# Kernel optimization log

Hardware: AMD Instinct MI355X
Metric: run time of the kernel (lower is better)

Reference implementation:

```python
import jax, jax.numpy as jnp
import numpy as np

ROI_SIZE = 7
N_ROIS = 64
H = W = 16
C = 2048


def _crop_resize(fm, box):
    """Crop fm[y1:y2, x1:x2] and bilinear-resize (TF2 half-pixel) to [S,S,C].
    fm: [H,W,C], box: [4] = (x1,y1,x2,y2) floats."""
    Hf, Wf = float(fm.shape[0]), float(fm.shape[1])
    S = ROI_SIZE
    x1 = jnp.maximum(0.0, jnp.round(box[0]))
    y1 = jnp.maximum(0.0, jnp.round(box[1]))
    x2 = jnp.minimum(Wf - 1.0, jnp.round(box[2]))
    y2 = jnp.minimum(Hf - 1.0, jnp.round(box[3]))
    h = y2 - y1  # crop is fm[y1:y2], i.e. height h
    w = x2 - x1
    # TF2 bilinear resize: half-pixel centers, coords relative to the crop
    iy = (jnp.arange(S, dtype=jnp.float32) + 0.5) * h / S - 0.5
    ix = (jnp.arange(S, dtype=jnp.float32) + 0.5) * w / S - 0.5
    iy = jnp.clip(iy, 0.0, h - 1.0)
    ix = jnp.clip(ix, 0.0, w - 1.0)
    y0 = jnp.floor(iy)
    x0 = jnp.floor(ix)
    fy = (iy - y0)[:, None, None]  # [S,1,1]
    fx = (ix - x0)[None, :, None]  # [1,S,1]
    y0i = (y1 + y0).astype(jnp.int32)
    y1i = jnp.minimum(y0i + 1, (y1 + h - 1.0).astype(jnp.int32))
    x0i = (x1 + x0).astype(jnp.int32)
    x1i = jnp.minimum(x0i + 1, (x1 + w - 1.0).astype(jnp.int32))
    top = jnp.take(fm, y0i, axis=0)   # [S,W,C]
    bot = jnp.take(fm, y1i, axis=0)
    rows = top * (1.0 - fy) + bot * fy
    left = jnp.take(rows, x0i, axis=1)   # [S,S,C]
    right = jnp.take(rows, x1i, axis=1)
    return left * (1.0 - fx) + right * fx


def setup_inputs() -> dict:
    key = jax.random.key(0)
    ks = jax.random.split(key, 8)
    feature_map = jax.random.normal(ks[0], (1, H, W, C), dtype=jnp.float32)
    # valid boxes: x1,y1 in [0,8), width/height in [2,7)
    lo = jax.random.uniform(ks[1], (N_ROIS, 2), minval=0.0, maxval=8.0)
    span = jax.random.uniform(ks[2], (N_ROIS, 2), minval=2.0, maxval=7.0)
    proposals = jnp.concatenate([lo, lo + span], axis=1)  # (x1,y1,x2,y2)
    D = ROI_SIZE * ROI_SIZE * C  # 100352
    W1 = jax.random.normal(ks[3], (D, 1024), dtype=jnp.float32) * 0.01
    b1 = jnp.zeros((1024,), jnp.float32)
    W2 = jax.random.normal(ks[4], (1024, 1024), dtype=jnp.float32) * 0.02
    b2 = jnp.zeros((1024,), jnp.float32)
    Wc = jax.random.normal(ks[5], (1024, 2), dtype=jnp.float32) * 0.02
    bc = jnp.zeros((2,), jnp.float32)
    Wb = jax.random.normal(ks[6], (1024, 4), dtype=jnp.float32) * 0.02
    bb = jnp.zeros((4,), jnp.float32)
    return {"feature_map": feature_map, "proposals": proposals,
            "W1": W1, "b1": b1, "W2": W2, "b2": b2,
            "Wc": Wc, "bc": bc, "Wb": Wb, "bb": bb}


def reference(feature_map, proposals, W1, b1, W2, b2, Wc, bc, Wb, bb):
    fm = feature_map[0]  # [H,W,C]
    rois = jax.vmap(lambda b: _crop_resize(fm, b))(proposals)  # [N,S,S,C]
    x = rois.reshape(proposals.shape[0], -1)                   # [N, S*S*C]
    x = jax.nn.relu(x @ W1 + b1)
    x = jax.nn.relu(x @ W2 + b2)
    cls_score = jax.nn.softmax(x @ Wc + bc, axis=-1)
    bbox_pred = x @ Wb + bb
    return cls_score, bbox_pred
```

## Files before the change

### kernel.cpp

```cpp
#include <hip/hip_runtime.h>
#include <math.h>

#define SS 7
#define NROIS 64
#define CC 2048
#define DD (SS*SS*CC)
#define MM 64
#define NN 1024
#define NP1 256
#define KC2 16
#define KCH2 64
#define W1COLS 512
#define WSTRIDE 520
#define FC1_LDS (32 * WSTRIDE * 4)

typedef float f32x4 __attribute__((ext_vector_type(4)));
typedef __bf16 bf16x8 __attribute__((ext_vector_type(8)));

#define LDS_BARRIER() do {                                         \
    asm volatile("s_waitcnt lgkmcnt(0)" ::: "memory");             \
    __builtin_amdgcn_s_barrier();                                  \
} while (0)

__device__ __forceinline__ unsigned short f2bf(float f){
    unsigned u = __builtin_bit_cast(unsigned, f);
    u += 0x7fffu + ((u >> 16) & 1u);
    return (unsigned short)(u >> 16);
}
__device__ __forceinline__ float bf2f(unsigned short h){
    unsigned u = ((unsigned)h) << 16;
    return __builtin_bit_cast(float, u);
}
__device__ __forceinline__ void splitpk(float v0, float v1, unsigned& h, unsigned& l){
    __bf16 h0 = (__bf16)v0, h1 = (__bf16)v1;
    float r0 = v0 - (float)h0, r1 = v1 - (float)h1;
    __bf16 l0 = (__bf16)r0, l1 = (__bf16)r1;
    h = (unsigned)__builtin_bit_cast(unsigned short, h0) |
        ((unsigned)__builtin_bit_cast(unsigned short, h1) << 16);
    l = (unsigned)__builtin_bit_cast(unsigned short, l0) |
        ((unsigned)__builtin_bit_cast(unsigned short, l1) << 16);
}


__global__ void crop_kernel(const float* __restrict__ fm,
                            const float* __restrict__ boxes,
                            unsigned short* __restrict__ XI) {
    int roi = blockIdx.x;
    int p   = blockIdx.y;
    int sy = p / SS, sx = p % SS;
    const float* b = boxes + roi * 4;
    float x1 = fmaxf(0.f, rintf(b[0]));
    float y1 = fmaxf(0.f, rintf(b[1]));
    float x2 = fminf(15.f, rintf(b[2]));
    float y2 = fminf(15.f, rintf(b[3]));
    float h = y2 - y1, w = x2 - x1;
    float iy = ((sy + 0.5f) * h) / 7.0f - 0.5f;
    float ix = ((sx + 0.5f) * w) / 7.0f - 0.5f;
    iy = fminf(fmaxf(iy, 0.f), h - 1.f);
    ix = fminf(fmaxf(ix, 0.f), w - 1.f);
    float y0 = floorf(iy), x0 = floorf(ix);
    float fy = iy - y0,   fx = ix - x0;
    int y0i = (int)(y1 + y0);
    int y1i = min(y0i + 1, (int)(y1 + h - 1.f));
    int x0i = (int)(x1 + x0);
    int x1i = min(x0i + 1, (int)(x1 + w - 1.f));

    int c = threadIdx.x * 4;
    const float4 v00 = *(const float4*)(fm + ((size_t)(y0i*16 + x0i))*CC + c);
    const float4 v01 = *(const float4*)(fm + ((size_t)(y0i*16 + x1i))*CC + c);
    const float4 v10 = *(const float4*)(fm + ((size_t)(y1i*16 + x0i))*CC + c);
    const float4 v11 = *(const float4*)(fm + ((size_t)(y1i*16 + x1i))*CC + c);
    float gy = 1.f - fy, gx = 1.f - fx;
    float o[4];
    o[0] = (v00.x*gy + v10.x*fy)*gx + (v01.x*gy + v11.x*fy)*fx;
    o[1] = (v00.y*gy + v10.y*fy)*gx + (v01.y*gy + v11.y*fy)*fx;
    o[2] = (v00.z*gy + v10.z*fy)*gx + (v01.z*gy + v11.z*fy)*fx;
    o[3] = (v00.w*gy + v10.w*fy)*gx + (v01.w*gy + v11.w*fy)*fx;
    uint2 hv, lv;
    splitpk(o[0], o[1], hv.x, lv.x);
    splitpk(o[2], o[3], hv.y, lv.y);
    int k = p * CC + c;
    size_t off = (size_t)roi * (2*DD) + (size_t)(k >> 3) * 16 + (k & 7);
    *(uint2*)(XI + off)     = hv;
    *(uint2*)(XI + off + 8) = lv;
}

__global__ __launch_bounds__(256, 2)
void fc1_gld(const unsigned short* __restrict__ AI,
             const float* __restrict__ Wm, float* __restrict__ P) {
    const int kc = blockIdx.x;
    const int nb = blockIdx.y;
    const int kt_cnt = 12 + (kc < 64 ? 1 : 0);
    const int k0 = (kc * 12 + (kc < 64 ? kc : 64)) * 32;

    const int t = threadIdx.x;
    const int lane = t & 63, wv = t >> 6;
    const int ln = lane & 15;
    const int koff = (lane >> 4) * 8;

    extern __shared__ float WS[];

    f32x4 acc[32];
    #pragma unroll
    for (int i = 0; i < 32; ++i) acc[i] = (f32x4){0.f, 0.f, 0.f, 0.f};

    size_t abase[4];
    #pragma unroll
    for (int mf = 0; mf < 4; ++mf)
        abase[mf] = (size_t)(mf * 16 + ln) * (2*DD) + (size_t)(k0 + koff) * 2;

    bf16x8 Ah[4], Al[4];

    const float* wtile = Wm + (size_t)k0 * NN + nb * W1COLS;

    for (int kt = 0; kt < kt_cnt; ++kt) {
        {
            const float* g0 = wtile + ((size_t)kt * 32 + wv * 8) * NN + (lane << 2);
            #pragma unroll
            for (int rr = 0; rr < 8; ++rr) {
                const float* g = g0 + (size_t)rr * NN;
                float* l = WS + (wv * 8 + rr) * WSTRIDE;
                __builtin_amdgcn_global_load_lds(
                    (const __attribute__((address_space(1))) void*)g,
                    (__attribute__((address_space(3))) void*)l, 16, 0, 0);
                __builtin_amdgcn_global_load_lds(
                    (const __attribute__((address_space(1))) void*)(g + 256),
                    (__attribute__((address_space(3))) void*)(l + 256), 16, 0, 0);
            }
        }
        #pragma unroll
        for (int mf = 0; mf < 4; ++mf) {
            Ah[mf] = *(const bf16x8*)(AI + abase[mf] + (size_t)kt * 64);
            Al[mf] = *(const bf16x8*)(AI + abase[mf] + (size_t)kt * 64 + 8);
        }
        __syncthreads();
        #pragma unroll
        for (int nf = 0; nf < 8; ++nf) {
            const int cb = koff * WSTRIDE + wv * 128 + nf * 16 + ln;
            float f0 = WS[cb + 0*WSTRIDE];
            float f1 = WS[cb + 1*WSTRIDE];
            float f2 = WS[cb + 2*WSTRIDE];
            float f3 = WS[cb + 3*WSTRIDE];
            float f4 = WS[cb + 4*WSTRIDE];
            float f5 = WS[cb + 5*WSTRIDE];
            float f6 = WS[cb + 6*WSTRIDE];
            float f7 = WS[cb + 7*WSTRIDE];
            unsigned h01,l01,h23,l23,h45,l45,h67,l67;
            splitpk(f0, f1, h01, l01);
            splitpk(f2, f3, h23, l23);
            splitpk(f4, f5, h45, l45);
            splitpk(f6, f7, h67, l67);
            typedef unsigned int uintx4 __attribute__((ext_vector_type(4)));
            bf16x8 Bh = __builtin_bit_cast(bf16x8, (uintx4){h01, h23, h45, h67});
            bf16x8 Bl = __builtin_bit_cast(bf16x8, (uintx4){l01, l23, l45, l67});
            #pragma unroll
            for (int mf = 0; mf < 4; ++mf) {
                acc[nf*4+mf] = __builtin_amdgcn_mfma_f32_16x16x32_bf16(Ah[mf], Bh, acc[nf*4+mf], 0, 0, 0);
                acc[nf*4+mf] = __builtin_amdgcn_mfma_f32_16x16x32_bf16(Ah[mf], Bl, acc[nf*4+mf], 0, 0, 0);
                acc[nf*4+mf] = __builtin_amdgcn_mfma_f32_16x16x32_bf16(Al[mf], Bh, acc[nf*4+mf], 0, 0, 0);
            }
        }
        __syncthreads();
    }

    const int orb = (lane >> 4) * 4;
    #pragma unroll
    for (int nf = 0; nf < 8; ++nf) {
        int col = nb * W1COLS + wv * 128 + nf * 16 + ln;
        #pragma unroll
        for (int mf = 0; mf < 4; ++mf) {
            #pragma unroll
            for (int i = 0; i < 4; ++i) {
                int m = mf * 16 + orb + i;
                P[((size_t)kc * MM + m) * NN + col] = acc[nf*4+mf][i];
            }
        }
    }
}

__global__ __launch_bounds__(256, 2)
void fc_mfma(const unsigned short* __restrict__ AI,
             const float* __restrict__ Wm, float* __restrict__ P,
             int rstride , int kchunk) {
    const int kc = blockIdx.x, nb = blockIdx.y;
    const int n0 = nb * 128;
    const int k0 = kc * kchunk;
    const int t = threadIdx.x;
    const int lane = t & 63, wv = t >> 6;
    const int ln = lane & 15;
    const int koff = (lane >> 4) * 8;
    const int kp = t & 15, no = t >> 4;

    __shared__ unsigned short WTh[128][34];
    __shared__ unsigned short WTl[128][34];

    f32x4 acc[8];
    #pragma unroll
    for (int i = 0; i < 8; ++i) acc[i] = (f32x4){0.f, 0.f, 0.f, 0.f};

    size_t abase[4];
    #pragma unroll
    for (int mf = 0; mf < 4; ++mf)
        abase[mf] = (size_t)(mf * 16 + ln) * rstride + (size_t)((k0 + koff) >> 3) * 16;

    const float* wbase = Wm + (size_t)k0 * NN + n0 + no * 8;

    float4 wa[4], wb[4];
    bf16x8 Aah[4], Aal[4], Abh[4], Abl[4];

    auto loadW = [&](int kt, float4* r) {
        const float* p = wbase + (size_t)(kt * 32 + 2 * kp) * NN;
        r[0] = *(const float4*)(p);
        r[1] = *(const float4*)(p + 4);
        r[2] = *(const float4*)(p + NN);
        r[3] = *(const float4*)(p + NN + 4);
    };
    auto loadA = [&](int kt, bf16x8* Ah, bf16x8* Al) {
        const size_t kb = (size_t)kt * 64;
        #pragma unroll
        for (int mf = 0; mf < 4; ++mf) {
            Ah[mf] = *(const bf16x8*)(AI + abase[mf] + kb);
            Al[mf] = *(const bf16x8*)(AI + abase[mf] + kb + 8);
        }
    };
    auto stageW = [&](const float4* r) {
        const float* r0 = (const float*)&r[0];
        const float* r1 = (const float*)&r[2];
        #pragma unroll
        for (int e = 0; e < 8; ++e) {
            int n = no * 8 + e;
            unsigned h, l;
            splitpk(r0[e], r1[e], h, l);
            *(unsigned*)&WTh[n][2 * kp] = h;
            *(unsigned*)&WTl[n][2 * kp] = l;
        }
    };

#define MFMA_PHASE(AH, AL)                                                     \
    {                                                                          \
        _Pragma("unroll")                                                      \
        for (int nf = 0; nf < 2; ++nf) {                                       \
            bf16x8 Bh = *(const bf16x8*)&WTh[wv * 32 + nf * 16 + ln][koff];    \
            bf16x8 Bl = *(const bf16x8*)&WTl[wv * 32 + nf * 16 + ln][koff];    \
            _Pragma("unroll")                                                  \
            for (int mf = 0; mf < 4; ++mf) {                                   \
                acc[nf*4+mf] = __builtin_amdgcn_mfma_f32_16x16x32_bf16(AH[mf], Bh, acc[nf*4+mf], 0, 0, 0); \
                acc[nf*4+mf] = __builtin_amdgcn_mfma_f32_16x16x32_bf16(AH[mf], Bl, acc[nf*4+mf], 0, 0, 0); \
                acc[nf*4+mf] = __builtin_amdgcn_mfma_f32_16x16x32_bf16(AL[mf], Bh, acc[nf*4+mf], 0, 0, 0); \
            }                                                                  \
        }                                                                      \
    }

    const int nkt = kchunk >> 5;
    loadW(0, wa);
    loadW(1, wb);
    loadA(0, Aah, Aal);
    loadA(1, Abh, Abl);

    for (int ktp = 0; ktp + 1 < nkt; ktp += 2) {
        LDS_BARRIER();
        stageW(wa);
        if (ktp + 2 < nkt) loadW(ktp + 2, wa);
        LDS_BARRIER();
        MFMA_PHASE(Aah, Aal);
        if (ktp + 2 < nkt) loadA(ktp + 2, Aah, Aal);
        LDS_BARRIER();
        stageW(wb);
        if (ktp + 3 < nkt) loadW(ktp + 3, wb);
        LDS_BARRIER();
        MFMA_PHASE(Abh, Abl);
        if (ktp + 3 < nkt) loadA(ktp + 3, Abh, Abl);
    }
    if (nkt & 1) {
        LDS_BARRIER();
        stageW(wa);
        LDS_BARRIER();
        MFMA_PHASE(Aah, Aal);
    }
#undef MFMA_PHASE

    const int orb = (lane >> 4) * 4;
    #pragma unroll
    for (int nf = 0; nf < 2; ++nf) {
        int col = n0 + wv * 32 + nf * 16 + ln;
        #pragma unroll
        for (int mf = 0; mf < 4; ++mf) {
            #pragma unroll
            for (int i = 0; i < 4; ++i) {
                int m = mf * 16 + orb + i;
                P[((size_t)kc * MM + m) * NN + col] = acc[nf*4+mf][i];
            }
        }
    }
}

__global__ void reduce_bias_split(const float* __restrict__ P,
                                  const float* __restrict__ bias,
                                  unsigned short* __restrict__ YI) {
    int idx = blockIdx.x * 256 + threadIdx.x;
    int n = idx & (NN - 1);
    int m = idx >> 10;
    float s0 = bias[n], s1 = 0.f, s2 = 0.f, s3 = 0.f;
    float s4 = 0.f, s5 = 0.f, s6 = 0.f, s7 = 0.f;
    for (int kc = 0; kc < NP1; kc += 8) {
        s0 += P[(size_t)(kc + 0) * (MM*NN) + idx];
        s1 += P[(size_t)(kc + 1) * (MM*NN) + idx];
        s2 += P[(size_t)(kc + 2) * (MM*NN) + idx];
        s3 += P[(size_t)(kc + 3) * (MM*NN) + idx];
        s4 += P[(size_t)(kc + 4) * (MM*NN) + idx];
        s5 += P[(size_t)(kc + 5) * (MM*NN) + idx];
        s6 += P[(size_t)(kc + 6) * (MM*NN) + idx];
        s7 += P[(size_t)(kc + 7) * (MM*NN) + idx];
    }
    float s = ((s0 + s1) + (s2 + s3)) + ((s4 + s5) + (s6 + s7));
    s = fmaxf(s, 0.f);
    unsigned short h = f2bf(s);
    size_t off = (size_t)m * (2*NN) + (size_t)(n >> 3) * 16 + (n & 7);
    YI[off]     = h;
    YI[off + 8] = f2bf(s - bf2f(h));
}

__global__ void heads_kernel(const float* __restrict__ P2,
                             const float* __restrict__ b2,
                             const float* __restrict__ Wc, const float* __restrict__ bc,
                             const float* __restrict__ Wb, const float* __restrict__ bb,
                             float* __restrict__ out) {
    int m = blockIdx.x;
    int t = threadIdx.x;
    float a[6] = {0,0,0,0,0,0};
    #pragma unroll
    for (int j = 0; j < 4; ++j) {
        int n = j * 256 + t;
        float s = b2[n];
        #pragma unroll
        for (int kc = 0; kc < KC2; ++kc)
            s += P2[((size_t)kc * MM + m) * NN + n];
        s = fmaxf(s, 0.f);
        a[0] += s * Wc[n*2 + 0];
        a[1] += s * Wc[n*2 + 1];
        a[2] += s * Wb[n*4 + 0];
        a[3] += s * Wb[n*4 + 1];
        a[4] += s * Wb[n*4 + 2];
        a[5] += s * Wb[n*4 + 3];
    }
    __shared__ float red[6][256];
    #pragma unroll
    for (int j = 0; j < 6; ++j) red[j][t] = a[j];
    __syncthreads();
    for (int s = 128; s > 0; s >>= 1) {
        if (t < s) {
            #pragma unroll
            for (int j = 0; j < 6; ++j) red[j][t] += red[j][t + s];
        }
        __syncthreads();
    }
    if (t == 0) {
        float l0 = red[0][0] + bc[0], l1 = red[1][0] + bc[1];
        float mx = fmaxf(l0, l1);
        float e0 = expf(l0 - mx), e1 = expf(l1 - mx);
        float inv = 1.f / (e0 + e1);
        out[m*2 + 0] = e0 * inv;
        out[m*2 + 1] = e1 * inv;
        out[128 + m*4 + 0] = red[2][0] + bb[0];
        out[128 + m*4 + 1] = red[3][0] + bb[1];
        out[128 + m*4 + 2] = red[4][0] + bb[2];
        out[128 + m*4 + 3] = red[5][0] + bb[3];
    }
}

extern "C" void kernel_launch(void* const* d_in, const int* in_sizes, int n_in,
                              void* d_out, int out_size, void* d_ws, size_t ws_size,
                              hipStream_t stream) {
    const float* fm    = (const float*)d_in[0];
    const float* boxes = (const float*)d_in[1];
    const float* W1    = (const float*)d_in[2];
    const float* b1    = (const float*)d_in[3];
    const float* W2    = (const float*)d_in[4];
    const float* b2    = (const float*)d_in[5];
    const float* Wc    = (const float*)d_in[6];
    const float* bc    = (const float*)d_in[7];
    const float* Wb    = (const float*)d_in[8];
    const float* bb    = (const float*)d_in[9];
    float* out = (float*)d_out;
    char* ws = (char*)d_ws;

    const size_t XIB = (size_t)NROIS * (2*DD) * sizeof(unsigned short);
    const size_t P1B = (size_t)NP1 * MM * NN * sizeof(float);
    unsigned short* XI  = (unsigned short*)ws;
    float*          P1  = (float*)(ws + XIB);
    unsigned short* h1I = (unsigned short*)(ws + XIB + P1B);
    float*          P2  = (float*)(ws + XIB + P1B + 262144);

    hipFuncSetAttribute((const void*)fc1_gld,
                        hipFuncAttributeMaxDynamicSharedMemorySize, FC1_LDS);

    crop_kernel<<<dim3(NROIS, SS*SS), 512, 0, stream>>>(fm, boxes, XI);
    fc1_gld<<<dim3(NP1, 2), 256, FC1_LDS, stream>>>(XI, W1, P1);
    reduce_bias_split<<<(MM*NN)/256, 256, 0, stream>>>(P1, b1, h1I);
    fc_mfma<<<dim3(KC2, 8), 256, 0, stream>>>(h1I, W2, P2, 2*NN, KCH2);
    heads_kernel<<<NROIS, 256, 0, stream>>>(P2, b2, Wc, bc, Wb, bb, out);
}
```

Measured before the change: 147.9 us.

## Double-buffer W1 tiles in fc1 and narrow column tile with longer K chunks

```diff
diff --git a/kernel.cpp b/kernel.cpp
--- a/kernel.cpp
+++ b/kernel.cpp
@@ -7,15 +7,16 @@
 #define DD (SS*SS*CC)
 #define MM 64
 #define NN 1024
-#define NP1 256
+#define NP1 128
 #define KC2 16
 #define KCH2 64
-#define W1COLS 512
-#define WSTRIDE 520
-#define FC1_LDS (32 * WSTRIDE * 4)
+#define W1COLS 256
+#define WSTRIDE 260
+#define FC1_LDS (2 * 32 * WSTRIDE * 4)
 
 typedef float f32x4 __attribute__((ext_vector_type(4)));
 typedef __bf16 bf16x8 __attribute__((ext_vector_type(8)));
+typedef unsigned int uintx4 __attribute__((ext_vector_type(4)));
 
 #define LDS_BARRIER() do {                                         \
     asm volatile("s_waitcnt lgkmcnt(0)" ::: "memory");             \
@@ -90,8 +91,8 @@
              const float* __restrict__ Wm, float* __restrict__ P) {
     const int kc = blockIdx.x;
     const int nb = blockIdx.y;
-    const int kt_cnt = 12 + (kc < 64 ? 1 : 0);
-    const int k0 = (kc * 12 + (kc < 64 ? kc : 64)) * 32;
+    const int kt_cnt = 24 + (kc < 64 ? 1 : 0);
+    const int k0 = (kc * 24 + (kc < 64 ? kc : 64)) * 32;
 
     const int t = threadIdx.x;
     const int lane = t & 63, wv = t >> 6;
@@ -100,9 +101,9 @@
 
     extern __shared__ float WS[];
 
-    f32x4 acc[32];
-    #pragma unroll
-    for (int i = 0; i < 32; ++i) acc[i] = (f32x4){0.f, 0.f, 0.f, 0.f};
+    f32x4 acc[16];
+    #pragma unroll
+    for (int i = 0; i < 16; ++i) acc[i] = (f32x4){0.f, 0.f, 0.f, 0.f};
 
     size_t abase[4];
     #pragma unroll
@@ -112,45 +113,46 @@
     bf16x8 Ah[4], Al[4];
 
     const float* wtile = Wm + (size_t)k0 * NN + nb * W1COLS;
+    auto issueW = [&](int kt, int buf) {
+        const float* g0 = wtile + ((size_t)kt * 32 + wv * 8) * NN + (lane << 2);
+        float* l0 = WS + buf * (32 * WSTRIDE) + (wv * 8) * WSTRIDE;
+        #pragma unroll
+        for (int rr = 0; rr < 8; ++rr) {
+            __builtin_amdgcn_global_load_lds(
+                (const __attribute__((address_space(1))) void*)(g0 + (size_t)rr * NN),
+                (__attribute__((address_space(3))) void*)(l0 + rr * WSTRIDE), 16, 0, 0);
+        }
+    };
+
+    issueW(0, 0);
 
     for (int kt = 0; kt < kt_cnt; ++kt) {
-        {
-            const float* g0 = wtile + ((size_t)kt * 32 + wv * 8) * NN + (lane << 2);
-            #pragma unroll
-            for (int rr = 0; rr < 8; ++rr) {
-                const float* g = g0 + (size_t)rr * NN;
-                float* l = WS + (wv * 8 + rr) * WSTRIDE;
-                __builtin_amdgcn_global_load_lds(
-                    (const __attribute__((address_space(1))) void*)g,
-                    (__attribute__((address_space(3))) void*)l, 16, 0, 0);
-                __builtin_amdgcn_global_load_lds(
-                    (const __attribute__((address_space(1))) void*)(g + 256),
-                    (__attribute__((address_space(3))) void*)(l + 256), 16, 0, 0);
-            }
-        }
+        const int cur = kt & 1;
         #pragma unroll
         for (int mf = 0; mf < 4; ++mf) {
             Ah[mf] = *(const bf16x8*)(AI + abase[mf] + (size_t)kt * 64);
             Al[mf] = *(const bf16x8*)(AI + abase[mf] + (size_t)kt * 64 + 8);
         }
-        __syncthreads();
-        #pragma unroll
-        for (int nf = 0; nf < 8; ++nf) {
-            const int cb = koff * WSTRIDE + wv * 128 + nf * 16 + ln;
-            float f0 = WS[cb + 0*WSTRIDE];
-            float f1 = WS[cb + 1*WSTRIDE];
-            float f2 = WS[cb + 2*WSTRIDE];
-            float f3 = WS[cb + 3*WSTRIDE];
-            float f4 = WS[cb + 4*WSTRIDE];
-            float f5 = WS[cb + 5*WSTRIDE];
-            float f6 = WS[cb + 6*WSTRIDE];
-            float f7 = WS[cb + 7*WSTRIDE];
+        if (kt + 1 < kt_cnt) issueW(kt + 1, 1 - cur);
+        asm volatile("s_waitcnt vmcnt(8)" ::: "memory");
+        __builtin_amdgcn_s_barrier();
+        const float* B = WS + cur * (32 * WSTRIDE);
+        #pragma unroll
+        for (int nf = 0; nf < 4; ++nf) {
+            const int cb = koff * WSTRIDE + wv * 64 + nf * 16 + ln;
+            float f0 = B[cb + 0*WSTRIDE];
+            float f1 = B[cb + 1*WSTRIDE];
+            float f2 = B[cb + 2*WSTRIDE];
+            float f3 = B[cb + 3*WSTRIDE];
+            float f4 = B[cb + 4*WSTRIDE];
+            float f5 = B[cb + 5*WSTRIDE];
+            float f6 = B[cb + 6*WSTRIDE];
+            float f7 = B[cb + 7*WSTRIDE];
             unsigned h01,l01,h23,l23,h45,l45,h67,l67;
             splitpk(f0, f1, h01, l01);
             splitpk(f2, f3, h23, l23);
             splitpk(f4, f5, h45, l45);
             splitpk(f6, f7, h67, l67);
-            typedef unsigned int uintx4 __attribute__((ext_vector_type(4)));
             bf16x8 Bh = __builtin_bit_cast(bf16x8, (uintx4){h01, h23, h45, h67});
             bf16x8 Bl = __builtin_bit_cast(bf16x8, (uintx4){l01, l23, l45, l67});
             #pragma unroll
@@ -160,13 +162,13 @@
                 acc[nf*4+mf] = __builtin_amdgcn_mfma_f32_16x16x32_bf16(Al[mf], Bh, acc[nf*4+mf], 0, 0, 0);
             }
         }
-        __syncthreads();
+        LDS_BARRIER();
     }
 
     const int orb = (lane >> 4) * 4;
     #pragma unroll
-    for (int nf = 0; nf < 8; ++nf) {
-        int col = nb * W1COLS + wv * 128 + nf * 16 + ln;
+    for (int nf = 0; nf < 4; ++nf) {
+        int col = nb * W1COLS + wv * 64 + nf * 16 + ln;
         #pragma unroll
         for (int mf = 0; mf < 4; ++mf) {
             #pragma unroll
@@ -395,7 +397,7 @@
                         hipFuncAttributeMaxDynamicSharedMemorySize, FC1_LDS);
 
     crop_kernel<<<dim3(NROIS, SS*SS), 512, 0, stream>>>(fm, boxes, XI);
-    fc1_gld<<<dim3(NP1, 2), 256, FC1_LDS, stream>>>(XI, W1, P1);
+    fc1_gld<<<dim3(NP1, 4), 256, FC1_LDS, stream>>>(XI, W1, P1);
     reduce_bias_split<<<(MM*NN)/256, 256, 0, stream>>>(P1, b1, h1I);
     fc_mfma<<<dim3(KC2, 8), 256, 0, stream>>>(h1I, W2, P2, 2*NN, KCH2);
     heads_kernel<<<NROIS, 256, 0, stream>>>(P2, b2, Wc, bc, Wb, bb, out);
```

Measured after the change: 131.8 us, median of 2. 10.9% less time.
